# Kernel optimization log

Measured on AMD Instinct MI355X. Metric: run time of the kernel, lower is better.

The kernel has to match this reference:

```python
import jax, jax.numpy as jnp
import numpy as np

B, FIN, NK, FOUT = 4096, 64, 512, 256

def setup_inputs() -> dict:
    key = jax.random.key(0)
    k1, k2, k3, k4 = jax.random.split(key, 4)
    input = jax.random.normal(k1, (B, FIN), dtype=jnp.float32)
    # xavier_uniform on [FOUT, NK]
    bound = float(np.sqrt(6.0 / (FOUT + NK)))
    weights = jax.random.uniform(k2, (FOUT, NK), minval=-bound, maxval=bound, dtype=jnp.float32)
    kernels_centers = jax.random.uniform(k3, (NK, FIN), minval=-1.0, maxval=1.0, dtype=jnp.float32)
    log_shapes = 0.1 * jax.random.normal(k4, (NK,), dtype=jnp.float32)
    return {"input": input, "weights": weights, "kernels_centers": kernels_centers, "log_shapes": log_shapes}

def reference(input, weights, kernels_centers, log_shapes):
    # diff: [B, NK, FIN]
    diff = input[:, None, :] - kernels_centers[None, :, :]
    # Euclidean norm over feature dim -> r: [B, NK]
    r = jnp.sqrt(jnp.sum(diff * diff, axis=-1))
    eps_r = jnp.exp(log_shapes)[None, :] * r
    # Gaussian radial function phi(x) = exp(-x^2)
    rbfs = jnp.exp(-(eps_r * eps_r))
    # normalization
    rbfs = rbfs / (1e-9 + jnp.sum(rbfs, axis=-1, keepdims=True))
    # out[b,o] = sum_k weights[o,k] * rbfs[b,k]
    out = jnp.einsum("ok,bk->bo", weights, rbfs)
    return out
```

## Files before the change

kernel.cpp:

```cpp
#include <hip/hip_runtime.h>
#include <math.h>

#define FIN   64
#define NK    512
#define FOUT  256
#define BB    16
#define NTHR  512
#define RSTRH 520

typedef __attribute__((ext_vector_type(8))) short short8;
typedef __attribute__((ext_vector_type(4))) float f32x4;

#define MFMA(a, b, c) __builtin_amdgcn_mfma_f32_16x16x32_bf16((a), (b), (c), 0, 0, 0)

__device__ __forceinline__ unsigned pack_hi16(float f0, float f1) {
    return __builtin_amdgcn_perm(__builtin_bit_cast(unsigned, f1),
                                 __builtin_bit_cast(unsigned, f0),
                                 0x07060302u);
}
__device__ __forceinline__ float trunc_bf(float f) {
    return __builtin_bit_cast(float, __builtin_bit_cast(unsigned, f) & 0xFFFF0000u);
}
__device__ __forceinline__ short8 split_step(float (&f)[8]) {
    union { unsigned u[4]; short8 s; } r;
    #pragma unroll
    for (int i = 0; i < 4; ++i) r.u[i] = pack_hi16(f[2 * i], f[2 * i + 1]);
    #pragma unroll
    for (int i = 0; i < 8; ++i) f[i] = f[i] - trunc_bf(f[i]);
    return r.s;
}
__device__ __forceinline__ short8 pack_bf(const float (&f)[8]) {
    union { unsigned u[4]; short8 s; } r;
    #pragma unroll
    for (int i = 0; i < 4; ++i) r.u[i] = pack_hi16(f[2 * i], f[2 * i + 1]);
    return r.s;
}
__device__ __forceinline__ void load8(const float* p, float (&f)[8]) {
    const float4 a = *(const float4*)p;
    const float4 b = *(const float4*)(p + 4);
    f[0] = a.x; f[1] = a.y; f[2] = a.z; f[3] = a.w;
    f[4] = b.x; f[5] = b.y; f[6] = b.z; f[7] = b.w;
}

__global__ __launch_bounds__(NTHR, 2) void rbf_fused_kernel(
    const float* __restrict__ x,
    const float* __restrict__ w,
    const float* __restrict__ cent,
    const float* __restrict__ ls,
    float* __restrict__ out)
{
    __shared__ float csqs[NK];
    __shared__ float e2s[NK];
    __shared__ float xsqs[BB];
    __shared__ float invs[BB];
    __shared__ float rowpart[8][BB];
    __shared__ __align__(16) unsigned short RsHi[BB][RSTRH];
    __shared__ __align__(16) unsigned short RsLo[BB][RSTRH];

    const int tid  = threadIdx.x;
    const int lane = tid & 63;
    const int wv   = tid >> 6;
    const int arow = lane & 15;
    const int d0   = (lane >> 4) * 8;
    const int b0   = blockIdx.x * BB;

    float xf0[8], xf1[8];
    {
        const float* xp = x + (size_t)(b0 + arow) * FIN;
        load8(xp + d0, xf0);
        load8(xp + 32 + d0, xf1);
    }
    {
        float q = 0.f;
        #pragma unroll
        for (int i = 0; i < 8; ++i) q = fmaf(xf0[i], xf0[i], fmaf(xf1[i], xf1[i], q));
        q += __shfl_xor(q, 16);
        q += __shfl_xor(q, 32);
        if (tid < BB) xsqs[tid] = q;
    }
    short8 ax1_0 = split_step(xf0), ax2_0 = split_step(xf0), ax3_0 = split_step(xf0);
    short8 ax1_1 = split_step(xf1), ax2_1 = split_step(xf1), ax3_1 = split_step(xf1);

    {
        const float* cp = cent + (size_t)tid * FIN;
        float cs = 0.f;
        #pragma unroll
        for (int j = 0; j < 16; ++j) {
            const float4 c4 = ((const float4*)cp)[j];
            cs = fmaf(c4.x, c4.x, cs); cs = fmaf(c4.y, c4.y, cs);
            cs = fmaf(c4.z, c4.z, cs); cs = fmaf(c4.w, c4.w, cs);
        }
        csqs[tid] = cs;
        e2s[tid]  = __expf(2.f * ls[tid]);
    }
    __syncthreads();

    float ps[4] = {0.f, 0.f, 0.f, 0.f};
    #pragma unroll 1
    for (int i = 0; i < 4; ++i) {
        const int n0 = 64 * wv + 16 * i;
        float cf0[8], cf1[8];
        {
            const float* cp = cent + (size_t)(n0 + arow) * FIN;
            load8(cp + d0, cf0);
            load8(cp + 32 + d0, cf1);
        }
        const short8 b1_0 = split_step(cf0), b2_0 = split_step(cf0), b3_0 = split_step(cf0);
        const short8 b1_1 = split_step(cf1), b2_1 = split_step(cf1), b3_1 = split_step(cf1);

        f32x4 acc = {0.f, 0.f, 0.f, 0.f};
        acc = MFMA(ax1_0, b1_0, acc);
        acc = MFMA(ax1_0, b2_0, acc);
        acc = MFMA(ax2_0, b1_0, acc);
        acc = MFMA(ax2_0, b2_0, acc);
        acc = MFMA(ax1_0, b3_0, acc);
        acc = MFMA(ax3_0, b1_0, acc);
        acc = MFMA(ax1_1, b1_1, acc);
        acc = MFMA(ax1_1, b2_1, acc);
        acc = MFMA(ax2_1, b1_1, acc);
        acc = MFMA(ax2_1, b2_1, acc);
        acc = MFMA(ax1_1, b3_1, acc);
        acc = MFMA(ax3_1, b1_1, acc);

        const int col = n0 + arow;
        const float cq = csqs[col];
        const float e2 = e2s[col];
        #pragma unroll
        for (int j = 0; j < 4; ++j) {
            const int row = (lane >> 4) * 4 + j;
            const float ssq = xsqs[row] + cq - 2.f * acc[j];
            const float rb  = __expf(-(e2 * ssq));
            ps[j] += rb;
            const float lo = rb - trunc_bf(rb);
            RsHi[row][col] = (unsigned short)(__builtin_bit_cast(unsigned, rb) >> 16);
            RsLo[row][col] = (unsigned short)(__builtin_bit_cast(unsigned, lo) >> 16);
        }
    }
    #pragma unroll
    for (int j = 0; j < 4; ++j) {
        float v = ps[j];
        v += __shfl_xor(v, 1);
        v += __shfl_xor(v, 2);
        v += __shfl_xor(v, 4);
        v += __shfl_xor(v, 8);
        if (arow == 0) rowpart[wv][(lane >> 4) * 4 + j] = v;
    }
    __syncthreads();
    if (tid < BB) {
        float s = 0.f;
        #pragma unroll
        for (int q = 0; q < 8; ++q) s += rowpart[q][tid];
        invs[tid] = 1.f / (1e-9f + s);
    }
    __syncthreads();

    const int n0 = 32 * wv;
    const float* wb0 = w + (size_t)(n0 + arow) * NK;
    const float* wb1 = w + (size_t)(n0 + 16 + arow) * NK;

    f32x4 o0 = {0.f, 0.f, 0.f, 0.f};
    f32x4 o1 = {0.f, 0.f, 0.f, 0.f};
    #pragma unroll 2
    for (int ks = 0; ks < NK / 32; ++ks) {
        const int kb = ks * 32 + d0;
        const short8 ahi = *(const short8*)&RsHi[arow][kb];
        const short8 alo = *(const short8*)&RsLo[arow][kb];
        float wf[8];
        load8(wb0 + kb, wf);
        {
            const short8 whi = split_step(wf);
            const short8 wlo = pack_bf(wf);
            o0 = MFMA(ahi, whi, o0);
            o0 = MFMA(ahi, wlo, o0);
            o0 = MFMA(alo, whi, o0);
        }
        load8(wb1 + kb, wf);
        {
            const short8 whi = split_step(wf);
            const short8 wlo = pack_bf(wf);
            o1 = MFMA(ahi, whi, o1);
            o1 = MFMA(ahi, wlo, o1);
            o1 = MFMA(alo, whi, o1);
        }
    }

    #pragma unroll
    for (int j = 0; j < 4; ++j) {
        const int row = (lane >> 4) * 4 + j;
        const float iv = invs[row];
        out[(size_t)(b0 + row) * FOUT + n0 + arow]      = o0[j] * iv;
        out[(size_t)(b0 + row) * FOUT + n0 + 16 + arow] = o1[j] * iv;
    }
}

extern "C" void kernel_launch(void* const* d_in, const int* in_sizes, int n_in,
                              void* d_out, int out_size, void* d_ws, size_t ws_size,
                              hipStream_t stream) {
    const float* x    = (const float*)d_in[0];
    const float* w    = (const float*)d_in[1];
    const float* cent = (const float*)d_in[2];
    const float* ls   = (const float*)d_in[3];
    float* out        = (float*)d_out;

    rbf_fused_kernel<<<dim3(4096 / BB), dim3(NTHR), 0, stream>>>(x, w, cent, ls, out);
}
```

Baseline: 83.55 us.

## Precompute bf16 splits of inputs, centers, weights in a prep kernel

Adds a prep kernel that splits x, centers and weights into bf16 hi/mid/lo planes in the workspace and precomputes squared norms and exp(2*log_shape). The main kernel then loads ready-made bf16 operands instead of re-splitting fp32 data in every block, which removes redundant conversion ALU work and halves weight bytes per block. The cost is an extra launch and a global round trip for the split data. The per-row epilogue is also unrolled with scalar accumulators.

```diff
diff --git a/kernel.cpp b/kernel.cpp
--- a/kernel.cpp
+++ b/kernel.cpp
@@ -10,103 +10,133 @@
 
 typedef __attribute__((ext_vector_type(8))) short short8;
 typedef __attribute__((ext_vector_type(4))) float f32x4;
+typedef unsigned short ushort_t;
 
 #define MFMA(a, b, c) __builtin_amdgcn_mfma_f32_16x16x32_bf16((a), (b), (c), 0, 0, 0)
 
-__device__ __forceinline__ unsigned pack_hi16(float f0, float f1) {
-    return __builtin_amdgcn_perm(__builtin_bit_cast(unsigned, f1),
-                                 __builtin_bit_cast(unsigned, f0),
-                                 0x07060302u);
+#define XHI   0
+#define XMID  262144
+#define XLO   524288
+#define CHI   786432
+#define CMID  819200
+#define CLO   851968
+#define WHI   884736
+#define WLO   1015808
+#define USH_END 1146880
+#define CSQ_F 0
+#define E2_F  512
+#define XSQ_F 1024
+
+__device__ __forceinline__ ushort_t top16(float f) {
+    return (ushort_t)(__builtin_bit_cast(unsigned, f) >> 16);
+}
+__device__ __forceinline__ float fromtop(ushort_t h) {
+    return __builtin_bit_cast(float, ((unsigned)h) << 16);
 }
 __device__ __forceinline__ float trunc_bf(float f) {
     return __builtin_bit_cast(float, __builtin_bit_cast(unsigned, f) & 0xFFFF0000u);
 }
-__device__ __forceinline__ short8 split_step(float (&f)[8]) {
-    union { unsigned u[4]; short8 s; } r;
-    #pragma unroll
-    for (int i = 0; i < 4; ++i) r.u[i] = pack_hi16(f[2 * i], f[2 * i + 1]);
-    #pragma unroll
-    for (int i = 0; i < 8; ++i) f[i] = f[i] - trunc_bf(f[i]);
-    return r.s;
-}
-__device__ __forceinline__ short8 pack_bf(const float (&f)[8]) {
-    union { unsigned u[4]; short8 s; } r;
-    #pragma unroll
-    for (int i = 0; i < 4; ++i) r.u[i] = pack_hi16(f[2 * i], f[2 * i + 1]);
-    return r.s;
-}
-__device__ __forceinline__ void load8(const float* p, float (&f)[8]) {
-    const float4 a = *(const float4*)p;
-    const float4 b = *(const float4*)(p + 4);
-    f[0] = a.x; f[1] = a.y; f[2] = a.z; f[3] = a.w;
-    f[4] = b.x; f[5] = b.y; f[6] = b.z; f[7] = b.w;
-}
-
-__global__ __launch_bounds__(NTHR, 2) void rbf_fused_kernel(
-    const float* __restrict__ x,
-    const float* __restrict__ w,
-    const float* __restrict__ cent,
-    const float* __restrict__ ls,
+
+__global__ __launch_bounds__(256) void rbf_prep_kernel(
+    const float* __restrict__ x, const float* __restrict__ w,
+    const float* __restrict__ cent, const float* __restrict__ ls,
+    ushort_t* __restrict__ us, float* __restrict__ fs)
+{
+    const int gid = blockIdx.x * 256 + threadIdx.x;
+    const int nth = gridDim.x * 256;
+
+    for (int i = gid; i < 4096 * FIN; i += nth) {
+        const float v = x[i];
+        const float m1 = v - trunc_bf(v);
+        const float l1 = m1 - trunc_bf(m1);
+        us[XHI + i]  = top16(v);
+        us[XMID + i] = top16(m1);
+        us[XLO + i]  = top16(l1);
+    }
+    for (int i = gid; i < NK * FIN; i += nth) {
+        const float v = cent[i];
+        const float m1 = v - trunc_bf(v);
+        const float l1 = m1 - trunc_bf(m1);
+        us[CHI + i]  = top16(v);
+        us[CMID + i] = top16(m1);
+        us[CLO + i]  = top16(l1);
+    }
+    for (int i = gid; i < FOUT * NK; i += nth) {
+        const float v = w[i];
+        const float l1 = v - trunc_bf(v);
+        us[WHI + i] = top16(v);
+        us[WLO + i] = top16(l1);
+    }
+    for (int r = gid; r < 4096; r += nth) {
+        const float4* xp = (const float4*)(x + (size_t)r * FIN);
+        float s = 0.f;
+        #pragma unroll
+        for (int j = 0; j < 16; ++j) {
+            const float4 c = xp[j];
+            s = fmaf(c.x, c.x, s); s = fmaf(c.y, c.y, s);
+            s = fmaf(c.z, c.z, s); s = fmaf(c.w, c.w, s);
+        }
+        fs[XSQ_F + r] = s;
+    }
+    for (int k = gid; k < NK; k += nth) {
+        const float4* cp = (const float4*)(cent + (size_t)k * FIN);
+        float s = 0.f;
+        #pragma unroll
+        for (int j = 0; j < 16; ++j) {
+            const float4 c = cp[j];
+            s = fmaf(c.x, c.x, s); s = fmaf(c.y, c.y, s);
+            s = fmaf(c.z, c.z, s); s = fmaf(c.w, c.w, s);
+        }
+        fs[CSQ_F + k] = s;
+        fs[E2_F + k]  = __expf(2.f * ls[k]);
+    }
+}
+
+__global__ __launch_bounds__(NTHR, 2) void rbf_main_kernel(
+    const ushort_t* __restrict__ us, const float* __restrict__ fs,
     float* __restrict__ out)
 {
-    __shared__ float csqs[NK];
-    __shared__ float e2s[NK];
-    __shared__ float xsqs[BB];
+    __shared__ __align__(16) ushort_t RsHi[BB][RSTRH];
+    __shared__ __align__(16) ushort_t RsLo[BB][RSTRH];
+    __shared__ float rowpart[8][BB];
     __shared__ float invs[BB];
-    __shared__ float rowpart[8][BB];
-    __shared__ __align__(16) unsigned short RsHi[BB][RSTRH];
-    __shared__ __align__(16) unsigned short RsLo[BB][RSTRH];
-
-    const int tid  = threadIdx.x;
-    const int lane = tid & 63;
-    const int wv   = tid >> 6;
-    const int arow = lane & 15;
-    const int d0   = (lane >> 4) * 8;
-    const int b0   = blockIdx.x * BB;
-
-    float xf0[8], xf1[8];
-    {
-        const float* xp = x + (size_t)(b0 + arow) * FIN;
-        load8(xp + d0, xf0);
-        load8(xp + 32 + d0, xf1);
-    }
-    {
-        float q = 0.f;
-        #pragma unroll
-        for (int i = 0; i < 8; ++i) q = fmaf(xf0[i], xf0[i], fmaf(xf1[i], xf1[i], q));
-        q += __shfl_xor(q, 16);
-        q += __shfl_xor(q, 32);
-        if (tid < BB) xsqs[tid] = q;
-    }
-    short8 ax1_0 = split_step(xf0), ax2_0 = split_step(xf0), ax3_0 = split_step(xf0);
-    short8 ax1_1 = split_step(xf1), ax2_1 = split_step(xf1), ax3_1 = split_step(xf1);
-
-    {
-        const float* cp = cent + (size_t)tid * FIN;
-        float cs = 0.f;
-        #pragma unroll
-        for (int j = 0; j < 16; ++j) {
-            const float4 c4 = ((const float4*)cp)[j];
-            cs = fmaf(c4.x, c4.x, cs); cs = fmaf(c4.y, c4.y, cs);
-            cs = fmaf(c4.z, c4.z, cs); cs = fmaf(c4.w, c4.w, cs);
-        }
-        csqs[tid] = cs;
-        e2s[tid]  = __expf(2.f * ls[tid]);
-    }
-    __syncthreads();
-
-    float ps[4] = {0.f, 0.f, 0.f, 0.f};
+
+    const int tid   = threadIdx.x;
+    const int lane  = tid & 63;
+    const int wv    = tid >> 6;
+    const int arow  = lane & 15;
+    const int dg    = lane >> 4;
+    const int d0    = dg * 8;
+    const int rbase = dg * 4;
+    const int b0    = blockIdx.x * BB;
+
+    const int xoff = (b0 + arow) * FIN;
+    const short8 ax1_0 = *(const short8*)&us[XHI  + xoff + d0];
+    const short8 ax1_1 = *(const short8*)&us[XHI  + xoff + 32 + d0];
+    const short8 ax2_0 = *(const short8*)&us[XMID + xoff + d0];
+    const short8 ax2_1 = *(const short8*)&us[XMID + xoff + 32 + d0];
+    const short8 ax3_0 = *(const short8*)&us[XLO  + xoff + d0];
+    const short8 ax3_1 = *(const short8*)&us[XLO  + xoff + 32 + d0];
+
+    const float xq0 = fs[XSQ_F + b0 + rbase + 0];
+    const float xq1 = fs[XSQ_F + b0 + rbase + 1];
+    const float xq2 = fs[XSQ_F + b0 + rbase + 2];
+    const float xq3 = fs[XSQ_F + b0 + rbase + 3];
+
+    float ps0 = 0.f, ps1 = 0.f, ps2 = 0.f, ps3 = 0.f;
     #pragma unroll 1
     for (int i = 0; i < 4; ++i) {
-        const int n0 = 64 * wv + 16 * i;
-        float cf0[8], cf1[8];
-        {
-            const float* cp = cent + (size_t)(n0 + arow) * FIN;
-            load8(cp + d0, cf0);
-            load8(cp + 32 + d0, cf1);
-        }
-        const short8 b1_0 = split_step(cf0), b2_0 = split_step(cf0), b3_0 = split_step(cf0);
-        const short8 b1_1 = split_step(cf1), b2_1 = split_step(cf1), b3_1 = split_step(cf1);
+        const int n0  = 64 * wv + 16 * i;
+        const int col = n0 + arow;
+        const int coff = col * FIN;
+        const short8 b1_0 = *(const short8*)&us[CHI  + coff + d0];
+        const short8 b1_1 = *(const short8*)&us[CHI  + coff + 32 + d0];
+        const short8 b2_0 = *(const short8*)&us[CMID + coff + d0];
+        const short8 b2_1 = *(const short8*)&us[CMID + coff + 32 + d0];
+        const short8 b3_0 = *(const short8*)&us[CLO  + coff + d0];
+        const short8 b3_1 = *(const short8*)&us[CLO  + coff + 32 + d0];
+        const float cq = fs[CSQ_F + col];
+        const float e2 = fs[E2_F + col];
 
         f32x4 acc = {0.f, 0.f, 0.f, 0.f};
         acc = MFMA(ax1_0, b1_0, acc);
@@ -122,28 +152,44 @@
         acc = MFMA(ax1_1, b3_1, acc);
         acc = MFMA(ax3_1, b1_1, acc);
 
-        const int col = n0 + arow;
-        const float cq = csqs[col];
-        const float e2 = e2s[col];
-        #pragma unroll
-        for (int j = 0; j < 4; ++j) {
-            const int row = (lane >> 4) * 4 + j;
-            const float ssq = xsqs[row] + cq - 2.f * acc[j];
-            const float rb  = __expf(-(e2 * ssq));
-            ps[j] += rb;
-            const float lo = rb - trunc_bf(rb);
-            RsHi[row][col] = (unsigned short)(__builtin_bit_cast(unsigned, rb) >> 16);
-            RsLo[row][col] = (unsigned short)(__builtin_bit_cast(unsigned, lo) >> 16);
-        }
-    }
-    #pragma unroll
-    for (int j = 0; j < 4; ++j) {
-        float v = ps[j];
-        v += __shfl_xor(v, 1);
-        v += __shfl_xor(v, 2);
-        v += __shfl_xor(v, 4);
-        v += __shfl_xor(v, 8);
-        if (arow == 0) rowpart[wv][(lane >> 4) * 4 + j] = v;
+        {
+            const float ssq = fmaf(-2.f, acc[0], xq0 + cq);
+            const float rb = __expf(-(e2 * ssq));
+            ps0 += rb;
+            RsHi[rbase + 0][col] = top16(rb);
+            RsLo[rbase + 0][col] = top16(rb - trunc_bf(rb));
+        }
+        {
+            const float ssq = fmaf(-2.f, acc[1], xq1 + cq);
+            const float rb = __expf(-(e2 * ssq));
+            ps1 += rb;
+            RsHi[rbase + 1][col] = top16(rb);
+            RsLo[rbase + 1][col] = top16(rb - trunc_bf(rb));
+        }
+        {
+            const float ssq = fmaf(-2.f, acc[2], xq2 + cq);
+            const float rb = __expf(-(e2 * ssq));
+            ps2 += rb;
+            RsHi[rbase + 2][col] = top16(rb);
+            RsLo[rbase + 2][col] = top16(rb - trunc_bf(rb));
+        }
+        {
+            const float ssq = fmaf(-2.f, acc[3], xq3 + cq);
+            const float rb = __expf(-(e2 * ssq));
+            ps3 += rb;
+            RsHi[rbase + 3][col] = top16(rb);
+            RsLo[rbase + 3][col] = top16(rb - trunc_bf(rb));
+        }
+    }
+    ps0 += __shfl_xor(ps0, 1); ps0 += __shfl_xor(ps0, 2); ps0 += __shfl_xor(ps0, 4); ps0 += __shfl_xor(ps0, 8);
+    ps1 += __shfl_xor(ps1, 1); ps1 += __shfl_xor(ps1, 2); ps1 += __shfl_xor(ps1, 4); ps1 += __shfl_xor(ps1, 8);
+    ps2 += __shfl_xor(ps2, 1); ps2 += __shfl_xor(ps2, 2); ps2 += __shfl_xor(ps2, 4); ps2 += __shfl_xor(ps2, 8);
+    ps3 += __shfl_xor(ps3, 1); ps3 += __shfl_xor(ps3, 2); ps3 += __shfl_xor(ps3, 4); ps3 += __shfl_xor(ps3, 8);
+    if (arow == 0) {
+        rowpart[wv][rbase + 0] = ps0;
+        rowpart[wv][rbase + 1] = ps1;
+        rowpart[wv][rbase + 2] = ps2;
+        rowpart[wv][rbase + 3] = ps3;
     }
     __syncthreads();
     if (tid < BB) {
@@ -154,9 +200,9 @@
     }
     __syncthreads();
 
-    const int n0 = 32 * wv;
-    const float* wb0 = w + (size_t)(n0 + arow) * NK;
-    const float* wb1 = w + (size_t)(n0 + 16 + arow) * NK;
+    const int c0 = 32 * wv;
+    const int w0off = (c0 + arow) * NK;
+    const int w1off = (c0 + 16 + arow) * NK;
 
     f32x4 o0 = {0.f, 0.f, 0.f, 0.f};
     f32x4 o1 = {0.f, 0.f, 0.f, 0.f};
@@ -165,31 +211,24 @@
         const int kb = ks * 32 + d0;
         const short8 ahi = *(const short8*)&RsHi[arow][kb];
         const short8 alo = *(const short8*)&RsLo[arow][kb];
-        float wf[8];
-        load8(wb0 + kb, wf);
-        {
-            const short8 whi = split_step(wf);
-            const short8 wlo = pack_bf(wf);
-            o0 = MFMA(ahi, whi, o0);
-            o0 = MFMA(ahi, wlo, o0);
-            o0 = MFMA(alo, whi, o0);
-        }
-        load8(wb1 + kb, wf);
-        {
-            const short8 whi = split_step(wf);
-            const short8 wlo = pack_bf(wf);
-            o1 = MFMA(ahi, whi, o1);
-            o1 = MFMA(ahi, wlo, o1);
-            o1 = MFMA(alo, whi, o1);
-        }
+        const short8 w0h = *(const short8*)&us[WHI + w0off + kb];
+        const short8 w0l = *(const short8*)&us[WLO + w0off + kb];
+        const short8 w1h = *(const short8*)&us[WHI + w1off + kb];
+        const short8 w1l = *(const short8*)&us[WLO + w1off + kb];
+        o0 = MFMA(ahi, w0h, o0);
+        o0 = MFMA(ahi, w0l, o0);
+        o0 = MFMA(alo, w0h, o0);
+        o1 = MFMA(ahi, w1h, o1);
+        o1 = MFMA(ahi, w1l, o1);
+        o1 = MFMA(alo, w1h, o1);
     }
 
     #pragma unroll
     for (int j = 0; j < 4; ++j) {
-        const int row = (lane >> 4) * 4 + j;
+        const int row = rbase + j;
         const float iv = invs[row];
-        out[(size_t)(b0 + row) * FOUT + n0 + arow]      = o0[j] * iv;
-        out[(size_t)(b0 + row) * FOUT + n0 + 16 + arow] = o1[j] * iv;
+        out[(size_t)(b0 + row) * FOUT + c0 + arow]      = o0[j] * iv;
+        out[(size_t)(b0 + row) * FOUT + c0 + 16 + arow] = o1[j] * iv;
     }
 }
 
@@ -202,5 +241,9 @@
     const float* ls   = (const float*)d_in[3];
     float* out        = (float*)d_out;
 
-    rbf_fused_kernel<<<dim3(4096 / BB), dim3(NTHR), 0, stream>>>(x, w, cent, ls, out);
-}
+    ushort_t* us = (ushort_t*)d_ws;
+    float*    fs = (float*)(us + USH_END);
+
+    rbf_prep_kernel<<<dim3(512), dim3(256), 0, stream>>>(x, w, cent, ls, us, fs);
+    rbf_main_kernel<<<dim3(4096 / BB), dim3(NTHR), 0, stream>>>(us, fs, out);
+}
```

Result: slower. 89.77 us (+7.4%).
